# Performance work log

Hardware: AMD Instinct MI355X
Metric: run time of the kernel (lower is better)

The kernel has to match this reference:

```python
import jax, jax.numpy as jnp
import numpy as np

BS, C_IN, C_OUT, K, STYLE_DIM, BANK = 8, 64, 64, 3, 512, 4
D = H = W = 32
EPS = 1e-8
STRIDE = 1
PAD = 1


def setup_inputs() -> dict:
    key = jax.random.key(0)
    ks = jax.random.split(key, 7)
    lim_f = 1.0 / np.sqrt(STYLE_DIM)
    return {
        "x": jax.random.normal(ks[0], (BS, C_IN, D, H, W), dtype=jnp.float32),
        "w": jax.random.normal(ks[1], (BS, STYLE_DIM), dtype=jnp.float32),
        "filter_w": jax.random.uniform(ks[2], (BANK, STYLE_DIM), jnp.float32, -lim_f, lim_f),
        "filter_b": jax.random.uniform(ks[3], (BANK,), jnp.float32, -lim_f, lim_f),
        "mod_w": jax.random.uniform(ks[4], (C_IN, STYLE_DIM), jnp.float32, -lim_f, lim_f),
        "mod_b": jax.random.uniform(ks[5], (C_IN,), jnp.float32, -lim_f, lim_f),
        "bank": jax.random.normal(ks[6], (BANK, C_OUT, C_IN, K, K, K), dtype=jnp.float32),
    }


def reference(x, w, filter_w, filter_b, mod_w, mod_b, bank):
    bs, c_in, d, h, ww = x.shape
    # bank selection weights: softmax over bank axis
    fwt = jax.nn.softmax(w @ filter_w.T + filter_b, axis=-1)          # [bs, bank]
    # per-sample weights from bank (bank layout: n, out, in, k, k, k)
    weighted = jnp.einsum('bn,noijkl->boijkl', fwt, bank)             # [bs, out, in, k, k, k]
    # style modulation over input channels
    mod = (w @ mod_w.T + mod_b).reshape(bs, 1, c_in, 1, 1, 1)
    mw = weighted * mod
    # demodulation: normalize each (sample, out-channel) filter
    demod = jax.lax.rsqrt(jnp.sum(mw * mw, axis=(2, 3, 4, 5), keepdims=True) + EPS)
    mw = mw * demod
    # grouped conv with groups = bs
    mw = mw.reshape(bs * C_OUT, c_in, K, K, K)
    xr = x.reshape(1, bs * c_in, d, h, ww)
    out = jax.lax.conv_general_dilated(
        xr, mw,
        window_strides=(STRIDE,) * 3,
        padding=[(PAD, PAD)] * 3,
        dimension_numbers=('NCDHW', 'OIDHW', 'NCDHW'),
        feature_group_count=bs,
    )
    return out.reshape(bs, C_OUT, out.shape[-3], out.shape[-2], out.shape[-1])
```

## Files before the change

### kernel.cpp

```cpp
#include <hip/hip_runtime.h>
#include <math.h>

#define BS 8
#define CIN 64
#define COUT 64
#define SDIM 512
#define NBANK 4
#define DSZ 32
#define SPATIAL (DSZ*DSZ*DSZ)
#define NTAP 27
#define CH 8
#define NCH 8
#define NST 14
#define SLABTEX (1124*33)
#define WINTEX 3301
#define XBUFT 3304
#define ABUFT 1792
#define XP_TEXELS (64*SLABTEX)
constexpr float EPS = 1e-8f;

typedef short bf16x8 __attribute__((ext_vector_type(8)));
typedef float f32x16 __attribute__((ext_vector_type(16)));

__device__ __forceinline__ unsigned pack2(float a, float b) {
    unsigned ua = __float_as_uint(a);
    unsigned ub = __float_as_uint(b);
    ua = (ua + 0x7fffu + ((ua >> 16) & 1u)) >> 16;
    ub = (ub + 0x7fffu + ((ub >> 16) & 1u)) & 0xffff0000u;
    return ua | ub;
}
__device__ __forceinline__ unsigned short bf16r(float f) {
    unsigned u = __float_as_uint(f);
    u = (u + 0x7fffu + ((u >> 16) & 1u)) >> 16;
    return (unsigned short)u;
}
__device__ __forceinline__ void gload_lds16(const int4* g, int4* l) {
    __builtin_amdgcn_global_load_lds(
        (const __attribute__((address_space(1))) unsigned int*)(const void*)g,
        (__attribute__((address_space(3))) unsigned int*)(void*)l, 16, 0, 0);
}

__global__ __launch_bounds__(256) void prep_fused(
        const float* __restrict__ x,
        const float* __restrict__ w,
        const float* __restrict__ filter_w,
        const float* __restrict__ filter_b,
        const float* __restrict__ mod_w,
        const float* __restrict__ mod_b,
        const float* __restrict__ bank,
        int4* __restrict__ xP,
        unsigned short* __restrict__ wA3) {
    const int gid = blockIdx.x;
    const int t   = threadIdx.x;

    if (gid < 128) {
        const int b   = gid >> 4;
        const int oc  = (gid & 15) * 4 + (t >> 6);
        const int ic  = t & 63;
        const float* wb = w + b * SDIM;

        float fw[NBANK];
#pragma unroll
        for (int n = 0; n < NBANK; ++n) {
            float p = 0.0f;
            const float* fr = filter_w + n * SDIM;
#pragma unroll
            for (int k = 0; k < 8; ++k) p += wb[ic + 64 * k] * fr[ic + 64 * k];
#pragma unroll
            for (int off = 32; off >= 1; off >>= 1) p += __shfl_xor(p, off, 64);
            fw[n] = p + filter_b[n];
        }
        float mx = fmaxf(fmaxf(fw[0], fw[1]), fmaxf(fw[2], fw[3]));
        float se = 0.0f;
#pragma unroll
        for (int n = 0; n < NBANK; ++n) { fw[n] = expf(fw[n] - mx); se += fw[n]; }
        const float inv = 1.0f / se;
        const float f0 = fw[0] * inv, f1 = fw[1] * inv, f2 = fw[2] * inv, f3 = fw[3] * inv;

        float m = mod_b[ic];
        {
            const float4* wv4 = (const float4*)wb;
            const float4* mr4 = (const float4*)(mod_w + ic * SDIM);
            for (int j = 0; j < SDIM / 4; ++j) {
                float4 a = wv4[j], c = mr4[j];
                m += a.x * c.x + a.y * c.y + a.z * c.z + a.w * c.w;
            }
        }

        const float* b0 = bank + (size_t)((0 * COUT + oc) * CIN + ic) * NTAP;
        const float* b1 = bank + (size_t)((1 * COUT + oc) * CIN + ic) * NTAP;
        const float* b2 = bank + (size_t)((2 * COUT + oc) * CIN + ic) * NTAP;
        const float* b3 = bank + (size_t)((3 * COUT + oc) * CIN + ic) * NTAP;

        float v[NTAP];
        float ss = 0.0f;
#pragma unroll
        for (int k = 0; k < NTAP; ++k) {
            float tv = f0 * b0[k] + f1 * b1[k] + f2 * b2[k] + f3 * b3[k];
            tv *= m;
            v[k] = tv;
            ss += tv * tv;
        }
#pragma unroll
        for (int off = 32; off >= 1; off >>= 1) ss += __shfl_xor(ss, off, 64);
        const float d = rsqrtf(ss + EPS);

        const int c_  = ic >> 3, icl = ic & 7;
        const int at_ = oc >> 5, ln_ = oc & 31;
        const size_t abase = (size_t)(b * NCH + c_) * NST * 128
                           + (size_t)at_ * 64 + ln_;
#pragma unroll
        for (int k = 0; k < NTAP; ++k) {
            const int dz = k / 9, r9 = k - dz * 9, dy = r9 / 3, dx = r9 - dy * 3;
            const int j  = dz * 3 + dx;
            int mm, hh;
            if (j < 8) { mm = 3 * (j >> 1) + dy; hh = j & 1; }
            else       { mm = (dy == 2) ? 13 : 12; hh = (dy == 1) ? 1 : 0; }
            const size_t tex = abase + (size_t)mm * 128 + (size_t)hh * 32;
            wA3[tex * 8 + icl] = bf16r(v[k] * d);
        }
        {
            const size_t tex = abase + (size_t)13 * 128 + 32;
            wA3[tex * 8 + icl] = 0;
        }
    } else {
        const int j2   = gid - 128;
        const int zidx = j2 % 34;
        const int ch   = (j2 / 34) & 7;
        const int b    = j2 / 272;
        int4* slab = xP + (size_t)(b * NCH + ch) * SLABTEX;
        const int4 z4 = make_int4(0, 0, 0, 0);

        if (zidx >= 32) {
            const int base = (zidx == 32) ? 0 : 1090 * 33;
            for (int p = t; p < 34 * 33; p += 256) slab[base + p] = z4;
            return;
        }
        const float* xc = x + ((size_t)b * CIN + ch * CH) * SPATIAL + zidx * 1024;
        int4* dst = slab + (34 + 33 * zidx) * 33;
        for (int p = t; p < 33 * 33; p += 256) {
            const int r  = p / 33;
            const int cx = p - r * 33;
            int4 vv = z4;
            if (r < 32 && cx > 0) {
                const float* s = xc + r * 32 + (cx - 1);
                vv.x = (int)pack2(s[0 * SPATIAL], s[1 * SPATIAL]);
                vv.y = (int)pack2(s[2 * SPATIAL], s[3 * SPATIAL]);
                vv.z = (int)pack2(s[4 * SPATIAL], s[5 * SPATIAL]);
                vv.w = (int)pack2(s[6 * SPATIAL], s[7 * SPATIAL]);
            }
            dst[p] = vv;
        }
    }
}

__global__ __launch_bounds__(512, 2) void conv3d_mfma(
        const int4* __restrict__ xP,
        const int4* __restrict__ wA3,
        float* __restrict__ out) {
    const int bid = blockIdx.x;
    const int b = bid & 7, z = bid >> 3;
    const int t    = threadIdx.x;
    const int l    = t & 63;
    const int ln31 = t & 31;
    const int h2   = (t >> 5) & 1;
    const int wv   = t >> 6;

    __shared__ int4 smem[2 * XBUFT + 2 * ABUFT];

    int rowQ[6];
#pragma unroll
    for (int q = 0; q < 6; ++q)
        rowQ[q] = ((wv * 4 + q) * 33 + ln31) * 16;
    int offc[4];
#pragma unroll
    for (int s = 0; s < 4; ++s) {
        const int j = 2 * s + h2;
        offc[s] = ((j / 3) * 1089 + (j % 3)) * 16;
    }
    const int off8 = (2 * 1089 + 2) * 16;

    auto stage = [&](int c, int buf) {
        const int4* xsrc = xP + (size_t)(b * NCH + c) * SLABTEX + (size_t)z * 1089;
        const int4* asrc = wA3 + (size_t)(b * NCH + c) * ABUFT;
        int4* lx = smem + buf * XBUFT;
        int4* la = smem + 2 * XBUFT + buf * ABUFT;
#pragma unroll
        for (int i = 0; i < 7; ++i) {
            const int p = i * 512 + t;
            if (p < WINTEX) gload_lds16(xsrc + p, lx + (p & ~63));
        }
#pragma unroll
        for (int i = 0; i < 4; ++i) {
            const int p = i * 512 + t;
            if (p < ABUFT) gload_lds16(asrc + p, la + (p & ~63));
        }
    };

    f32x16 acc[2][4];
#pragma unroll
    for (int i = 0; i < 2; ++i)
#pragma unroll
        for (int j = 0; j < 4; ++j)
#pragma unroll
            for (int r = 0; r < 16; ++r) acc[i][j][r] = 0.0f;

    stage(0, 0);
    __syncthreads();

    for (int c = 0; c < NCH; ++c) {
        if (c + 1 < NCH) stage(c + 1, (c + 1) & 1);
        const char* Xb = (const char*)(smem + (c & 1) * XBUFT);
        const char* Ab = (const char*)(smem + 2 * XBUFT + (c & 1) * ABUFT);

        auto mfma4 = [&](const bf16x8& a, const int4& Bf, int at) {
        };
        (void)mfma4;

#pragma unroll
        for (int s = 0; s < 4; ++s) {
            int4 F[6];
#pragma unroll
            for (int q = 0; q < 6; ++q)
                F[q] = *(const int4*)(Xb + rowQ[q] + offc[s]);
            bf16x8 a0[2], a1[2], a2[2];
#pragma unroll
            for (int at = 0; at < 2; ++at) {
                a0[at] = *(const bf16x8*)(Ab + (3 * s + 0) * 2048 + at * 1024 + l * 16);
                a1[at] = *(const bf16x8*)(Ab + (3 * s + 1) * 2048 + at * 1024 + l * 16);
                a2[at] = *(const bf16x8*)(Ab + (3 * s + 2) * 2048 + at * 1024 + l * 16);
            }
#pragma unroll
            for (int at = 0; at < 2; ++at)
#pragma unroll
                for (int st = 0; st < 4; ++st)
                    acc[at][st] = __builtin_amdgcn_mfma_f32_32x32x16_bf16(
                        a0[at], *(const bf16x8*)&F[st], acc[at][st], 0, 0, 0);
#pragma unroll
            for (int at = 0; at < 2; ++at)
#pragma unroll
                for (int st = 0; st < 4; ++st)
                    acc[at][st] = __builtin_amdgcn_mfma_f32_32x32x16_bf16(
                        a1[at], *(const bf16x8*)&F[st + 1], acc[at][st], 0, 0, 0);
#pragma unroll
            for (int at = 0; at < 2; ++at)
#pragma unroll
                for (int st = 0; st < 4; ++st)
                    acc[at][st] = __builtin_amdgcn_mfma_f32_32x32x16_bf16(
                        a2[at], *(const bf16x8*)&F[st + 2], acc[at][st], 0, 0, 0);
        }

        {
            int4 T1[4], T2[4];
#pragma unroll
            for (int st = 0; st < 4; ++st) {
                T1[st] = *(const int4*)(Xb + rowQ[st] + h2 * (33 * 16) + off8);
                T2[st] = *(const int4*)(Xb + rowQ[st + 2] + off8);
            }
            bf16x8 a12[2], a13[2];
#pragma unroll
            for (int at = 0; at < 2; ++at) {
                a12[at] = *(const bf16x8*)(Ab + 12 * 2048 + at * 1024 + l * 16);
                a13[at] = *(const bf16x8*)(Ab + 13 * 2048 + at * 1024 + l * 16);
            }
#pragma unroll
            for (int at = 0; at < 2; ++at)
#pragma unroll
                for (int st = 0; st < 4; ++st)
                    acc[at][st] = __builtin_amdgcn_mfma_f32_32x32x16_bf16(
                        a12[at], *(const bf16x8*)&T1[st], acc[at][st], 0, 0, 0);
#pragma unroll
            for (int at = 0; at < 2; ++at)
#pragma unroll
                for (int st = 0; st < 4; ++st)
                    acc[at][st] = __builtin_amdgcn_mfma_f32_32x32x16_bf16(
                        a13[at], *(const bf16x8*)&T2[st], acc[at][st], 0, 0, 0);
        }
        __syncthreads();
    }

    float* ob = out + (size_t)b * COUT * SPATIAL + (size_t)z * 1024;
#pragma unroll
    for (int at = 0; at < 2; ++at)
#pragma unroll
        for (int st = 0; st < 4; ++st) {
            const int sp = (wv * 4 + st) * 32 + ln31;
#pragma unroll
            for (int r = 0; r < 16; ++r) {
                const int oc = at * 32 + (r & 3) + 8 * (r >> 2) + 4 * h2;
                ob[(size_t)oc * SPATIAL + sp] = acc[at][st][r];
            }
        }
}

extern "C" void kernel_launch(void* const* d_in, const int* in_sizes, int n_in,
                              void* d_out, int out_size, void* d_ws, size_t ws_size,
                              hipStream_t stream) {
    const float* x        = (const float*)d_in[0];
    const float* w        = (const float*)d_in[1];
    const float* filter_w = (const float*)d_in[2];
    const float* filter_b = (const float*)d_in[3];
    const float* mod_w    = (const float*)d_in[4];
    const float* mod_b    = (const float*)d_in[5];
    const float* bank     = (const float*)d_in[6];
    float* out = (float*)d_out;

    int4* xP = (int4*)d_ws;
    unsigned short* wA3 = (unsigned short*)(xP + XP_TEXELS);

    prep_fused<<<128 + 34 * 8 * 8, 256, 0, stream>>>(
        x, w, filter_w, filter_b, mod_w, mod_b, bank, xP, wA3);
    conv3d_mfma<<<256, 512, 0, stream>>>(xP, (const int4*)wA3, out);
}
```

Baseline: 84.58 us.

## Split conv output channels across wave pairs with 1024-thread blocks

The conv kernel doubles block size to 1024 threads, and each wave now computes only one 32-wide output-channel half instead of both. Accumulators per thread drop from 8 to 4 MFMA tiles, which lowers register pressure and doubles waves per block to hide latency. In exchange, each X fragment is read from LDS by two waves instead of one, so LDS traffic per MFMA rises. Block-level barriers now also span twice as many waves.

```diff
diff --git a/kernel.cpp b/kernel.cpp
--- a/kernel.cpp
+++ b/kernel.cpp
@@ -154,7 +154,7 @@
     }
 }
 
-__global__ __launch_bounds__(512, 2) void conv3d_mfma(
+__global__ __launch_bounds__(1024, 4) void conv3d_mfma(
         const int4* __restrict__ xP,
         const int4* __restrict__ wA3,
         float* __restrict__ out) {
@@ -165,13 +165,15 @@
     const int ln31 = t & 31;
     const int h2   = (t >> 5) & 1;
     const int wv   = t >> 6;
+    const int oh   = wv & 1;
+    const int rg   = wv >> 1;
 
     __shared__ int4 smem[2 * XBUFT + 2 * ABUFT];
 
     int rowQ[6];
 #pragma unroll
     for (int q = 0; q < 6; ++q)
-        rowQ[q] = ((wv * 4 + q) * 33 + ln31) * 16;
+        rowQ[q] = ((rg * 4 + q) * 33 + ln31) * 16;
     int offc[4];
 #pragma unroll
     for (int s = 0; s < 4; ++s) {
@@ -186,24 +188,22 @@
         int4* lx = smem + buf * XBUFT;
         int4* la = smem + 2 * XBUFT + buf * ABUFT;
 #pragma unroll
-        for (int i = 0; i < 7; ++i) {
-            const int p = i * 512 + t;
+        for (int i = 0; i < 4; ++i) {
+            const int p = i * 1024 + t;
             if (p < WINTEX) gload_lds16(xsrc + p, lx + (p & ~63));
         }
 #pragma unroll
-        for (int i = 0; i < 4; ++i) {
-            const int p = i * 512 + t;
+        for (int i = 0; i < 2; ++i) {
+            const int p = i * 1024 + t;
             if (p < ABUFT) gload_lds16(asrc + p, la + (p & ~63));
         }
     };
 
-    f32x16 acc[2][4];
-#pragma unroll
-    for (int i = 0; i < 2; ++i)
-#pragma unroll
-        for (int j = 0; j < 4; ++j)
-#pragma unroll
-            for (int r = 0; r < 16; ++r) acc[i][j][r] = 0.0f;
+    f32x16 acc[4];
+#pragma unroll
+    for (int j = 0; j < 4; ++j)
+#pragma unroll
+        for (int r = 0; r < 16; ++r) acc[j][r] = 0.0f;
 
     stage(0, 0);
     __syncthreads();
@@ -213,41 +213,21 @@
         const char* Xb = (const char*)(smem + (c & 1) * XBUFT);
         const char* Ab = (const char*)(smem + 2 * XBUFT + (c & 1) * ABUFT);
 
-        auto mfma4 = [&](const bf16x8& a, const int4& Bf, int at) {
-        };
-        (void)mfma4;
-
 #pragma unroll
         for (int s = 0; s < 4; ++s) {
             int4 F[6];
 #pragma unroll
             for (int q = 0; q < 6; ++q)
                 F[q] = *(const int4*)(Xb + rowQ[q] + offc[s]);
-            bf16x8 a0[2], a1[2], a2[2];
-#pragma unroll
-            for (int at = 0; at < 2; ++at) {
-                a0[at] = *(const bf16x8*)(Ab + (3 * s + 0) * 2048 + at * 1024 + l * 16);
-                a1[at] = *(const bf16x8*)(Ab + (3 * s + 1) * 2048 + at * 1024 + l * 16);
-                a2[at] = *(const bf16x8*)(Ab + (3 * s + 2) * 2048 + at * 1024 + l * 16);
-            }
-#pragma unroll
-            for (int at = 0; at < 2; ++at)
+#pragma unroll
+            for (int dy = 0; dy < 3; ++dy) {
+                const bf16x8 a = *(const bf16x8*)(
+                    Ab + (3 * s + dy) * 2048 + oh * 1024 + l * 16);
 #pragma unroll
                 for (int st = 0; st < 4; ++st)
-                    acc[at][st] = __builtin_amdgcn_mfma_f32_32x32x16_bf16(
-                        a0[at], *(const bf16x8*)&F[st], acc[at][st], 0, 0, 0);
-#pragma unroll
-            for (int at = 0; at < 2; ++at)
-#pragma unroll
-                for (int st = 0; st < 4; ++st)
-                    acc[at][st] = __builtin_amdgcn_mfma_f32_32x32x16_bf16(
-                        a1[at], *(const bf16x8*)&F[st + 1], acc[at][st], 0, 0, 0);
-#pragma unroll
-            for (int at = 0; at < 2; ++at)
-#pragma unroll
-                for (int st = 0; st < 4; ++st)
-                    acc[at][st] = __builtin_amdgcn_mfma_f32_32x32x16_bf16(
-                        a2[at], *(const bf16x8*)&F[st + 2], acc[at][st], 0, 0, 0);
+                    acc[st] = __builtin_amdgcn_mfma_f32_32x32x16_bf16(
+                        a, *(const bf16x8*)&F[st + dy], acc[st], 0, 0, 0);
+            }
         }
 
         {
@@ -257,40 +237,30 @@
                 T1[st] = *(const int4*)(Xb + rowQ[st] + h2 * (33 * 16) + off8);
                 T2[st] = *(const int4*)(Xb + rowQ[st + 2] + off8);
             }
-            bf16x8 a12[2], a13[2];
-#pragma unroll
-            for (int at = 0; at < 2; ++at) {
-                a12[at] = *(const bf16x8*)(Ab + 12 * 2048 + at * 1024 + l * 16);
-                a13[at] = *(const bf16x8*)(Ab + 13 * 2048 + at * 1024 + l * 16);
-            }
-#pragma unroll
-            for (int at = 0; at < 2; ++at)
-#pragma unroll
-                for (int st = 0; st < 4; ++st)
-                    acc[at][st] = __builtin_amdgcn_mfma_f32_32x32x16_bf16(
-                        a12[at], *(const bf16x8*)&T1[st], acc[at][st], 0, 0, 0);
-#pragma unroll
-            for (int at = 0; at < 2; ++at)
-#pragma unroll
-                for (int st = 0; st < 4; ++st)
-                    acc[at][st] = __builtin_amdgcn_mfma_f32_32x32x16_bf16(
-                        a13[at], *(const bf16x8*)&T2[st], acc[at][st], 0, 0, 0);
+            const bf16x8 a12 = *(const bf16x8*)(Ab + 12 * 2048 + oh * 1024 + l * 16);
+            const bf16x8 a13 = *(const bf16x8*)(Ab + 13 * 2048 + oh * 1024 + l * 16);
+#pragma unroll
+            for (int st = 0; st < 4; ++st)
+                acc[st] = __builtin_amdgcn_mfma_f32_32x32x16_bf16(
+                    a12, *(const bf16x8*)&T1[st], acc[st], 0, 0, 0);
+#pragma unroll
+            for (int st = 0; st < 4; ++st)
+                acc[st] = __builtin_amdgcn_mfma_f32_32x32x16_bf16(
+                    a13, *(const bf16x8*)&T2[st], acc[st], 0, 0, 0);
         }
         __syncthreads();
     }
 
     float* ob = out + (size_t)b * COUT * SPATIAL + (size_t)z * 1024;
 #pragma unroll
-    for (int at = 0; at < 2; ++at)
-#pragma unroll
-        for (int st = 0; st < 4; ++st) {
-            const int sp = (wv * 4 + st) * 32 + ln31;
-#pragma unroll
-            for (int r = 0; r < 16; ++r) {
-                const int oc = at * 32 + (r & 3) + 8 * (r >> 2) + 4 * h2;
-                ob[(size_t)oc * SPATIAL + sp] = acc[at][st][r];
-            }
-        }
+    for (int st = 0; st < 4; ++st) {
+        const int sp = (rg * 4 + st) * 32 + ln31;
+#pragma unroll
+        for (int r = 0; r < 16; ++r) {
+            const int oc = oh * 32 + (r & 3) + 8 * (r >> 2) + 4 * h2;
+            ob[(size_t)oc * SPATIAL + sp] = acc[st][r];
+        }
+    }
 }
 
 extern "C" void kernel_launch(void* const* d_in, const int* in_sizes, int n_in,
@@ -310,5 +280,5 @@
 
     prep_fused<<<128 + 34 * 8 * 8, 256, 0, stream>>>(
         x, w, filter_w, filter_b, mod_w, mod_b, bank, xP, wA3);
-    conv3d_mfma<<<256, 512, 0, stream>>>(xP, (const int4*)wA3, out);
-}
+    conv3d_mfma<<<256, 1024, 0, stream>>>(xP, (const int4*)wA3, out);
+}
```

Measured after the change: 89.63 us. 1.06x slower.
